# Kernel optimization log

Hardware: AMD Instinct MI355X
Metric: run time of the kernel (lower is better)

Reference implementation:

```python
import jax, jax.numpy as jnp
import numpy as np

B, S, D = 2, 2048, 1024
H = 16
DK = D // H  # 64

def setup_inputs() -> dict:
    key = jax.random.key(0)
    ks = jax.random.split(key, 7)
    scale = 1.0 / np.sqrt(D)
    return {
        "Query": jax.random.normal(ks[0], (B, S, D), dtype=jnp.float32),
        "Key":   jax.random.normal(ks[1], (B, S, D), dtype=jnp.float32),
        "Value": jax.random.normal(ks[2], (B, S, D), dtype=jnp.float32),
        "Wq": jax.random.normal(ks[3], (D, D), dtype=jnp.float32) * scale,
        "Wk": jax.random.normal(ks[4], (D, D), dtype=jnp.float32) * scale,
        "Wv": jax.random.normal(ks[5], (D, D), dtype=jnp.float32) * scale,
        "Wo": jax.random.normal(ks[6], (D, D), dtype=jnp.float32) * scale,
    }

def reference(Query, Key, Value, Wq, Wk, Wv, Wo):
    b = Query.shape[0]
    # nn.Linear(bias=False): x @ W.T ; reshape to [B, H, S, DK]
    q = (Query @ Wq.T).reshape(b, -1, H, DK).transpose(0, 2, 1, 3)
    k = (Key   @ Wk.T).reshape(b, -1, H, DK).transpose(0, 2, 1, 3)
    v = (Value @ Wv.T).reshape(b, -1, H, DK).transpose(0, 2, 1, 3)
    # full O(S^2) score matrix [B, H, Sq, Sk]
    scores = jnp.einsum("bhqd,bhkd->bhqk", q, k) / jnp.sqrt(jnp.float32(DK))
    # FAITHFUL to source: nn.Softmax(dim=1) normalizes over the HEAD axis
    attn = jax.nn.softmax(scores, axis=1)
    ctx = jnp.einsum("bhqk,bhkd->bhqd", attn, v)  # [B, H, Sq, DK]
    ctx = ctx.transpose(0, 2, 1, 3).reshape(b, -1, H * DK)  # [B, S, D]
    return ctx @ Wo.T
```

## Files before the change

### kernel.cpp

```cpp
#include <hip/hip_runtime.h>
#include <stdint.h>

#define BB   2
#define SS   2048
#define DD   1024
#define HH   16
#define DKK  64
#define MM   (BB*SS)

typedef __attribute__((ext_vector_type(4))) float f32x4;
typedef __attribute__((ext_vector_type(8))) short s16x8;

#define MFMA_B16(a, b, c) __builtin_amdgcn_mfma_f32_16x16x32_bf16((a), (b), (c), 0, 0, 0)

__device__ __forceinline__ ushort f2bf(float f) {
  uint u = __float_as_uint(f);
  u += 0x7FFFu + ((u >> 16) & 1u);
  return (ushort)(u >> 16);
}
__device__ __forceinline__ float bf2f(ushort u) {
  return __uint_as_float((uint)u << 16);
}
#if __has_builtin(__builtin_amdgcn_exp2f)
#define EXP2(x) __builtin_amdgcn_exp2f(x)
#else
#define EXP2(x) exp2f(x)
#endif

__device__ __forceinline__ s16x8 cvt8(const float* src) {
  float4 a = *(const float4*)src, b = *(const float4*)(src + 4);
  union { uint u[4]; s16x8 v; } r;
  asm("v_cvt_pk_bf16_f32 %0, %1, %2" : "=v"(r.u[0]) : "v"(a.x), "v"(a.y));
  asm("v_cvt_pk_bf16_f32 %0, %1, %2" : "=v"(r.u[1]) : "v"(a.z), "v"(a.w));
  asm("v_cvt_pk_bf16_f32 %0, %1, %2" : "=v"(r.u[2]) : "v"(b.x), "v"(b.y));
  asm("v_cvt_pk_bf16_f32 %0, %1, %2" : "=v"(r.u[3]) : "v"(b.z), "v"(b.w));
  return r.v;
}

#define QSCALE (0.125f * 1.4426950408889634f)

__global__ void cvt_kernel(const float* __restrict__ src, ushort* __restrict__ dst, int n) {
  int i = (blockIdx.x * 256 + threadIdx.x) * 8;
  if (i >= n) return;
  *(s16x8*)(dst + i) = cvt8(src + i);
}

__global__ __launch_bounds__(256, 2) void qkv_proj(
    const float* __restrict__ Ia, const float* __restrict__ Ib, const float* __restrict__ Ic,
    const ushort* __restrict__ Wa, const ushort* __restrict__ Wb, const ushort* __restrict__ Wc,
    ushort* __restrict__ Oa, ushort* __restrict__ Ob, ushort* __restrict__ Oc)
{
  __shared__ ushort As[128 * 32];
  __shared__ ushort Bs[128 * 32];
  const int tid  = threadIdx.x;
  const int lane = tid & 63, wave = tid >> 6;
  const int q = lane & 15, g = lane >> 4;
  const int wr = wave >> 1, wc = wave & 1;
  const int mblk = blockIdx.x * 128, nblk = blockIdx.y * 128;
  const int mode = blockIdx.z;

  const float*  A = (mode == 0) ? Ia : (mode == 1) ? Ib : Ic;
  const ushort* W = (mode == 0) ? Wa : (mode == 1) ? Wb : Wc;

  f32x4 acc[4][4];
  {
    f32x4 z = {0.f, 0.f, 0.f, 0.f};
#pragma unroll
    for (int i = 0; i < 4; ++i)
#pragma unroll
      for (int j = 0; j < 4; ++j) acc[i][j] = z;
  }

  const int r0 = tid >> 2;
  const int e0 = (tid & 3) * 8;
  for (int k0 = 0; k0 < 1024; k0 += 32) {
#pragma unroll
    for (int it = 0; it < 2; ++it) {
      const int row = r0 + it * 64;
      *(s16x8*)&As[row * 32 + e0] = cvt8(A + (size_t)(mblk + row) * 1024 + k0 + e0);
      *(s16x8*)&Bs[row * 32 + e0] = *(const s16x8*)(W + (size_t)(nblk + row) * 1024 + k0 + e0);
    }
    __syncthreads();
    s16x8 af[4], bf[4];
#pragma unroll
    for (int t = 0; t < 4; ++t) {
      af[t] = *(const s16x8*)&As[(wr * 64 + t * 16 + q) * 32 + g * 8];
      bf[t] = *(const s16x8*)&Bs[(wc * 64 + t * 16 + q) * 32 + g * 8];
    }
#pragma unroll
    for (int mt = 0; mt < 4; ++mt)
#pragma unroll
      for (int nt = 0; nt < 4; ++nt)
        acc[mt][nt] = MFMA_B16(af[mt], bf[nt], acc[mt][nt]);
    __syncthreads();
  }

  if (mode == 2) {
    ushort* Vt = Oc;
#pragma unroll
    for (int mt = 0; mt < 4; ++mt)
#pragma unroll
      for (int nt = 0; nt < 4; ++nt) {
        const int s0 = mblk + wr * 64 + mt * 16 + g * 4;
        const int o  = nblk + wc * 64 + nt * 16 + q;
        const int h = o >> 6, dk = o & 63;
        const int b = s0 >> 11, sr = s0 & 2047;
        ushort4 pk;
        pk.x = f2bf(acc[mt][nt][0]); pk.y = f2bf(acc[mt][nt][1]);
        pk.z = f2bf(acc[mt][nt][2]); pk.w = f2bf(acc[mt][nt][3]);
        *(ushort4*)(Vt + ((size_t)((b * 16 + h) * 64 + dk)) * SS + sr) = pk;
      }
  } else {
    const float scale = (mode == 0) ? QSCALE : 1.0f;
    ushort* P = (mode == 0) ? Oa : Ob;
    ushort* wl = As + wave * 1024;
    const int h0 = (nblk + wc * 64) >> 6;
#pragma unroll
    for (int mt = 0; mt < 4; ++mt) {
      const int s0 = mblk + wr * 64 + mt * 16;
      const int b  = s0 >> 11, sr0 = s0 & 2047;
#pragma unroll
      for (int nt = 0; nt < 4; ++nt)
#pragma unroll
        for (int j = 0; j < 4; ++j)
          wl[(g * 4 + j) * 64 + nt * 16 + q] = f2bf(acc[mt][nt][j] * scale);
#pragma unroll
      for (int it = 0; it < 2; ++it) {
        s16x8 v = *(const s16x8*)((char*)wl + it * 1024 + lane * 16);
        const int lr = it * 8 + (lane >> 3);
        const int c  = (lane & 7) * 8;
        *(s16x8*)(P + ((size_t)((b * 16 + h0) * SS) + sr0 + lr) * DKK + c) = v;
      }
    }
  }
}

__global__ __launch_bounds__(256, 2) void o_proj(
    const ushort* __restrict__ A, const ushort* __restrict__ W,
    float* __restrict__ O)
{
  __shared__ ushort As[128 * 32];
  __shared__ ushort Bs[128 * 32];
  const int tid  = threadIdx.x;
  const int lane = tid & 63, wave = tid >> 6;
  const int q = lane & 15, g = lane >> 4;
  const int wr = wave >> 1, wc = wave & 1;
  const int mblk = blockIdx.x * 128, nblk = blockIdx.y * 128;

  f32x4 acc[4][4];
  {
    f32x4 z = {0.f, 0.f, 0.f, 0.f};
#pragma unroll
    for (int i = 0; i < 4; ++i)
#pragma unroll
      for (int j = 0; j < 4; ++j) acc[i][j] = z;
  }

  const int r0 = tid >> 2;
  const int e0 = (tid & 3) * 8;
  for (int k0 = 0; k0 < 1024; k0 += 32) {
#pragma unroll
    for (int it = 0; it < 2; ++it) {
      const int row = r0 + it * 64;
      *(s16x8*)&As[row * 32 + e0] = *(const s16x8*)(A + (size_t)(mblk + row) * 1024 + k0 + e0);
      *(s16x8*)&Bs[row * 32 + e0] = *(const s16x8*)(W + (size_t)(nblk + row) * 1024 + k0 + e0);
    }
    __syncthreads();
    s16x8 af[4], bf[4];
#pragma unroll
    for (int t = 0; t < 4; ++t) {
      af[t] = *(const s16x8*)&As[(wr * 64 + t * 16 + q) * 32 + g * 8];
      bf[t] = *(const s16x8*)&Bs[(wc * 64 + t * 16 + q) * 32 + g * 8];
    }
#pragma unroll
    for (int mt = 0; mt < 4; ++mt)
#pragma unroll
      for (int nt = 0; nt < 4; ++nt)
        acc[mt][nt] = MFMA_B16(af[mt], bf[nt], acc[mt][nt]);
    __syncthreads();
  }

#pragma unroll
  for (int mt = 0; mt < 4; ++mt)
#pragma unroll
    for (int nt = 0; nt < 4; ++nt)
#pragma unroll
      for (int j = 0; j < 4; ++j) {
        const int s = mblk + wr * 64 + mt * 16 + g * 4 + j;
        const int o = nblk + wc * 64 + nt * 16 + q;
        O[(size_t)s * DD + o] = acc[mt][nt][j];
      }
}

__global__ __launch_bounds__(256, 2) void den_kernel(
    const ushort* __restrict__ Qp, const ushort* __restrict__ Kp,
    ushort* __restrict__ Rden)
{
  __shared__ ushort smem[2][16384];
  const int tid  = threadIdx.x;
  const int lane = tid & 63, wave = tid >> 6;
  const int q = lane & 15, g = lane >> 4;
  const int wr = wave >> 1, wc = wave & 1;
  const int kblk = blockIdx.x * 128, qblk = blockIdx.y * 128;
  const int b = blockIdx.z;

  f32x4 den[4][4];
  {
    f32x4 z = {0.f, 0.f, 0.f, 0.f};
#pragma unroll
    for (int i = 0; i < 4; ++i)
#pragma unroll
      for (int j = 0; j < 4; ++j) den[i][j] = z;
  }

  const int srow = tid >> 3, sseg = tid & 7;
  const int sd   = (sseg * 8) ^ ((srow & 7) << 3);

  const ushort* Kb0 = Kp + ((size_t)(b * 16) * SS + kblk) * DKK;
  const ushort* Qb0 = Qp + ((size_t)(b * 16) * SS + qblk) * DKK;

#pragma unroll
  for (int i = 0; i < 4; ++i) {
    const int row = srow + i * 32;
    *(s16x8*)&smem[0][row * 64 + sd]        = *(const s16x8*)(Kb0 + (size_t)row * DKK + sseg * 8);
    *(s16x8*)&smem[0][8192 + row * 64 + sd] = *(const s16x8*)(Qb0 + (size_t)row * DKK + sseg * 8);
  }
  __syncthreads();

  for (int s = 0; s < 16; ++s) {
    const int cur = s & 1;
    s16x8 nA[4], nB[4];
    if (s < 15) {
      const ushort* Kh = Kb0 + (size_t)(s + 1) * SS * DKK;
      const ushort* Qh = Qb0 + (size_t)(s + 1) * SS * DKK;
#pragma unroll
      for (int i = 0; i < 4; ++i) {
        const int row = srow + i * 32;
        nA[i] = *(const s16x8*)(Kh + (size_t)row * DKK + sseg * 8);
        nB[i] = *(const s16x8*)(Qh + (size_t)row * DKK + sseg * 8);
      }
    }
    s16x8 af[4][2], bf[4][2];
#pragma unroll
    for (int t = 0; t < 4; ++t) {
      const int ra = wr * 64 + t * 16 + q;
      const int rb = wc * 64 + t * 16 + q;
      af[t][0] = *(const s16x8*)&smem[cur][ra * 64 + ((g * 8) ^ ((ra & 7) << 3))];
      af[t][1] = *(const s16x8*)&smem[cur][ra * 64 + ((32 + g * 8) ^ ((ra & 7) << 3))];
      bf[t][0] = *(const s16x8*)&smem[cur][8192 + rb * 64 + ((g * 8) ^ ((rb & 7) << 3))];
      bf[t][1] = *(const s16x8*)&smem[cur][8192 + rb * 64 + ((32 + g * 8) ^ ((rb & 7) << 3))];
    }
#pragma unroll
    for (int mt = 0; mt < 4; ++mt)
#pragma unroll
      for (int nt = 0; nt < 4; ++nt) {
        f32x4 c = {0.f, 0.f, 0.f, 0.f};
        c = MFMA_B16(af[mt][0], bf[nt][0], c);
        c = MFMA_B16(af[mt][1], bf[nt][1], c);
#pragma unroll
        for (int r = 0; r < 4; ++r)
          den[mt][nt][r] += EXP2(c[r]);
      }
    if (s < 15) {
#pragma unroll
      for (int i = 0; i < 4; ++i) {
        const int row = srow + i * 32;
        *(s16x8*)&smem[cur ^ 1][row * 64 + sd]        = nA[i];
        *(s16x8*)&smem[cur ^ 1][8192 + row * 64 + sd] = nB[i];
      }
    }
    __syncthreads();
  }

  char* aw2 = (char*)smem + wave * 8192;
#pragma unroll
  for (int mt = 0; mt < 4; ++mt)
#pragma unroll
    for (int nt = 0; nt < 4; ++nt) {
      const int ql = nt * 16 + q;
      const float i0 = 1.0f / den[mt][nt][0], i1 = 1.0f / den[mt][nt][1];
      const float i2 = 1.0f / den[mt][nt][2], i3 = 1.0f / den[mt][nt][3];
      uint2 pk;
      asm("v_cvt_pk_bf16_f32 %0, %1, %2" : "=v"(pk.x) : "v"(i0), "v"(i1));
      asm("v_cvt_pk_bf16_f32 %0, %1, %2" : "=v"(pk.y) : "v"(i2), "v"(i3));
      *(uint2*)(aw2 + ql * 128 + ((mt * 32 + g * 8) ^ ((ql & 7) << 4))) = pk;
    }
#pragma unroll
  for (int it = 0; it < 8; ++it) {
    const int idx = it * 64 + lane;
    const int row = idx >> 3;
    const int seg = idx & 7;
    s16x8 v = *(const s16x8*)(aw2 + row * 128 + ((seg * 16) ^ ((row & 7) << 4)));
    *(s16x8*)(Rden + (size_t)b * SS * SS
              + (size_t)(qblk + wc * 64 + row) * SS
              + kblk + wr * 64 + seg * 8) = v;
  }
}

__global__ __launch_bounds__(512, 2) void attn5_kernel(
    const ushort* __restrict__ Qp, const ushort* __restrict__ Kp,
    const ushort* __restrict__ Vt, const ushort* __restrict__ Rden,
    ushort* __restrict__ Ctx)
{
  __shared__ ushort Ktile[2][64 * 64];
  __shared__ ushort Vtile[2][64 * 64];
  __shared__ ushort Rw_all[8][16 * 64];
  __shared__ ushort aw_all[8][16 * 64];

  const int tid  = threadIdx.x;
  const int lane = tid & 63;
  const int w    = tid >> 6;
  const int q    = lane & 15;
  const int g    = lane >> 4;
  const int bid  = blockIdx.x;
  const int bh   = bid & 31;
  const int b    = bh >> 4, h = bh & 15;
  const int qblk = (bid >> 5) * 128;

  const ushort* Qb = Qp + ((size_t)bh * SS + qblk + w * 16 + q) * DKK + g * 8;
  s16x8 qf0 = *(const s16x8*)(Qb);
  s16x8 qf1 = *(const s16x8*)(Qb + 32);

  const ushort* Ks = Kp + (size_t)bh * SS * DKK;
  const ushort* Vs = Vt + (size_t)bh * DKK * SS;
  const ushort* Rs = Rden + (size_t)b * SS * SS + (size_t)(qblk + w * 16) * SS;

  f32x4 acc[4];
  {
    f32x4 z = {0.f, 0.f, 0.f, 0.f};
#pragma unroll
    for (int n = 0; n < 4; ++n) acc[n] = z;
  }

  ushort* Rw = Rw_all[w];
  ushort* aw = aw_all[w];
  const int srow = tid >> 3, sseg = tid & 7;
  const int sd   = (sseg * 8) ^ ((srow & 7) << 3);
  const int r16  = lane >> 2;
  const int sgA  = (lane & 3) * 2;
  const int rd0  = r16 * 64 + ((sgA * 8) ^ ((r16 & 7) << 3));
  const int rd1  = r16 * 64 + (((sgA + 1) * 8) ^ ((r16 & 7) << 3));

  {
    s16x8 gK  = *(const s16x8*)(Ks + tid * 8);
    s16x8 gV  = *(const s16x8*)(Vs + (size_t)srow * SS + sseg * 8);
    s16x8 gR0 = *(const s16x8*)(Rs + (size_t)r16 * SS + sgA * 8);
    s16x8 gR1 = *(const s16x8*)(Rs + (size_t)r16 * SS + (sgA + 1) * 8);
    *(s16x8*)&Ktile[0][srow * 64 + sd] = gK;
    *(s16x8*)&Vtile[0][srow * 64 + sd] = gV;
    *(s16x8*)&Rw[rd0] = gR0;
    *(s16x8*)&Rw[rd1] = gR1;
  }
  __syncthreads();

  for (int kt = 0; kt < 32; ++kt) {
    const int cur = kt & 1;
    s16x8 gK, gV, gR0, gR1;
    if (kt < 31) {
      const int k1 = (kt + 1) * 64;
      gK  = *(const s16x8*)(Ks + (size_t)k1 * DKK + tid * 8);
      gV  = *(const s16x8*)(Vs + (size_t)srow * SS + k1 + sseg * 8);
      gR0 = *(const s16x8*)(Rs + (size_t)r16 * SS + k1 + sgA * 8);
      gR1 = *(const s16x8*)(Rs + (size_t)r16 * SS + k1 + (sgA + 1) * 8);
    }
    const ushort* Kt = Ktile[cur];
    const ushort* Vv = Vtile[cur];

#pragma unroll
    for (int ks = 0; ks < 4; ++ks) {
      const int kr = ks * 16 + q;
      s16x8 a0 = *(const s16x8*)&Kt[kr * 64 + ((g * 8) ^ ((kr & 7) << 3))];
      s16x8 a1 = *(const s16x8*)&Kt[kr * 64 + ((32 + g * 8) ^ ((kr & 7) << 3))];
      f32x4 c = {0.f, 0.f, 0.f, 0.f};
      c = MFMA_B16(a0, qf0, c);
      c = MFMA_B16(a1, qf1, c);
      ushort4 rv = *(const ushort4*)&Rw[q * 64 + (((ks * 2 + (g >> 1)) ^ (q & 7)) * 8) + (g & 1) * 4];
      float p0 = EXP2(c[0]) * bf2f(rv.x);
      float p1 = EXP2(c[1]) * bf2f(rv.y);
      float p2 = EXP2(c[2]) * bf2f(rv.z);
      float p3 = EXP2(c[3]) * bf2f(rv.w);
      uint2 pp;
      asm("v_cvt_pk_bf16_f32 %0, %1, %2" : "=v"(pp.x) : "v"(p0), "v"(p1));
      asm("v_cvt_pk_bf16_f32 %0, %1, %2" : "=v"(pp.y) : "v"(p2), "v"(p3));
      *(uint2*)&aw[q * 64 + ((ks * 16 + g * 4) ^ ((q & 7) << 3))] = pp;
    }
#pragma unroll
    for (int kc = 0; kc < 2; ++kc) {
      s16x8 vf[4];
#pragma unroll
      for (int n = 0; n < 4; ++n) {
        const int vr = n * 16 + q;
        vf[n] = *(const s16x8*)&Vv[vr * 64 + ((kc * 32 + g * 8) ^ ((vr & 7) << 3))];
      }
      s16x8 pa = *(const s16x8*)&aw[q * 64 + ((kc * 32 + g * 8) ^ ((q & 7) << 3))];
#pragma unroll
      for (int n = 0; n < 4; ++n)
        acc[n] = MFMA_B16(pa, vf[n], acc[n]);
    }
    if (kt < 31) {
      *(s16x8*)&Ktile[cur ^ 1][srow * 64 + sd] = gK;
      *(s16x8*)&Vtile[cur ^ 1][srow * 64 + sd] = gV;
      *(s16x8*)&Rw[rd0] = gR0;
      *(s16x8*)&Rw[rd1] = gR1;
    }
    __syncthreads();
  }

#pragma unroll
  for (int n = 0; n < 4; ++n)
#pragma unroll
    for (int j = 0; j < 4; ++j)
      aw[(g * 4 + j) * 64 + n * 16 + q] = f2bf(acc[n][j]);
  ushort* P = Ctx + ((size_t)(b * SS) + qblk + w * 16) * DD + h * 64;
#pragma unroll
  for (int it = 0; it < 2; ++it) {
    const int idx = it * 64 + lane;
    const int row = idx >> 3;
    const int seg = idx & 7;
    s16x8 v = *(const s16x8*)&aw[row * 64 + seg * 8];
    *(s16x8*)(P + (size_t)row * DD + seg * 8) = v;
  }
}

extern "C" void kernel_launch(void* const* d_in, const int* in_sizes, int n_in,
                              void* d_out, int out_size, void* d_ws, size_t ws_size,
                              hipStream_t stream) {
  const float* Query = (const float*)d_in[0];
  const float* Key   = (const float*)d_in[1];
  const float* Value = (const float*)d_in[2];
  const float* Wq    = (const float*)d_in[3];
  const float* Wk    = (const float*)d_in[4];
  const float* Wv    = (const float*)d_in[5];
  const float* Wo    = (const float*)d_in[6];

  size_t off = 0;
  char* ws = (char*)d_ws;
  auto alloc = [&](size_t bytes) -> void* {
    void* p = ws + off;
    off += (bytes + 255) & ~(size_t)255;
    return p;
  };
  const size_t nX = (size_t)MM * DD;
  const size_t nW = (size_t)DD * DD;
  const size_t nS = (size_t)BB * SS * SS;
  ushort* Wqb  = (ushort*)alloc(nW * 2);
  ushort* Wkb  = (ushort*)alloc(nW * 2);
  ushort* Wvb  = (ushort*)alloc(nW * 2);
  ushort* Wob  = (ushort*)alloc(nW * 2);
  ushort* Qp   = (ushort*)alloc(nX * 2);
  ushort* Kp   = (ushort*)alloc(nX * 2);
  ushort* Vtb  = (ushort*)alloc(nX * 2);
  ushort* Rden = (ushort*)alloc(nS * 2);
  ushort* Ctx  = (ushort*)alloc(nX * 2);

  cvt_kernel<<<(int)(nW / 2048), 256, 0, stream>>>(Wq, Wqb, (int)nW);
  cvt_kernel<<<(int)(nW / 2048), 256, 0, stream>>>(Wk, Wkb, (int)nW);
  cvt_kernel<<<(int)(nW / 2048), 256, 0, stream>>>(Wv, Wvb, (int)nW);
  cvt_kernel<<<(int)(nW / 2048), 256, 0, stream>>>(Wo, Wob, (int)nW);

  qkv_proj<<<dim3(32, 8, 3), 256, 0, stream>>>(
      Query, Key, Value, Wqb, Wkb, Wvb, Qp, Kp, Vtb);

  den_kernel<<<dim3(16, 16, 2), 256, 0, stream>>>(Qp, Kp, Rden);
  attn5_kernel<<<512, 512, 0, stream>>>(Qp, Kp, Vtb, Rden, Ctx);

  o_proj<<<dim3(32, 8), 256, 0, stream>>>(Ctx, Wob, (float*)d_out);
}
```

Measured before the change: 162.6 us.

## Double-buffer LDS tiles in QKV projection GEMM with register prefetch

The QKV projection main loop now uses two LDS buffers per operand. Global loads for the next K-slice are issued into registers before the MFMAs on the current slice, then converted and stored into the alternate buffer afterward. This hides global memory latency behind compute and removes one barrier per iteration. In exchange it doubles LDS use and raises register pressure, which could hurt occupancy under the 2-blocks-per-CU launch bound.

Measured after the change: 162.8 us. No clear change (+0.1%).

```diff
diff --git a/kernel.cpp b/kernel.cpp
--- a/kernel.cpp
+++ b/kernel.cpp
@@ -27,8 +27,7 @@
 #define EXP2(x) exp2f(x)
 #endif
 
-__device__ __forceinline__ s16x8 cvt8(const float* src) {
-  float4 a = *(const float4*)src, b = *(const float4*)(src + 4);
+__device__ __forceinline__ s16x8 pack8(float4 a, float4 b) {
   union { uint u[4]; s16x8 v; } r;
   asm("v_cvt_pk_bf16_f32 %0, %1, %2" : "=v"(r.u[0]) : "v"(a.x), "v"(a.y));
   asm("v_cvt_pk_bf16_f32 %0, %1, %2" : "=v"(r.u[1]) : "v"(a.z), "v"(a.w));
@@ -36,6 +35,9 @@
   asm("v_cvt_pk_bf16_f32 %0, %1, %2" : "=v"(r.u[3]) : "v"(b.z), "v"(b.w));
   return r.v;
 }
+__device__ __forceinline__ s16x8 cvt8(const float* src) {
+  return pack8(*(const float4*)src, *(const float4*)(src + 4));
+}
 
 #define QSCALE (0.125f * 1.4426950408889634f)
 
@@ -50,8 +52,8 @@
     const ushort* __restrict__ Wa, const ushort* __restrict__ Wb, const ushort* __restrict__ Wc,
     ushort* __restrict__ Oa, ushort* __restrict__ Ob, ushort* __restrict__ Oc)
 {
-  __shared__ ushort As[128 * 32];
-  __shared__ ushort Bs[128 * 32];
+  __shared__ ushort As[2][128 * 32];
+  __shared__ ushort Bs[2][128 * 32];
   const int tid  = threadIdx.x;
   const int lane = tid & 63, wave = tid >> 6;
   const int q = lane & 15, g = lane >> 4;
@@ -73,25 +75,49 @@
 
   const int r0 = tid >> 2;
   const int e0 = (tid & 3) * 8;
-  for (int k0 = 0; k0 < 1024; k0 += 32) {
-#pragma unroll
-    for (int it = 0; it < 2; ++it) {
-      const int row = r0 + it * 64;
-      *(s16x8*)&As[row * 32 + e0] = cvt8(A + (size_t)(mblk + row) * 1024 + k0 + e0);
-      *(s16x8*)&Bs[row * 32 + e0] = *(const s16x8*)(W + (size_t)(nblk + row) * 1024 + k0 + e0);
-    }
-    __syncthreads();
+
+#pragma unroll
+  for (int it = 0; it < 2; ++it) {
+    const int row = r0 + it * 64;
+    *(s16x8*)&As[0][row * 32 + e0] = cvt8(A + (size_t)(mblk + row) * 1024 + e0);
+    *(s16x8*)&Bs[0][row * 32 + e0] = *(const s16x8*)(W + (size_t)(nblk + row) * 1024 + e0);
+  }
+  __syncthreads();
+
+  for (int s = 0; s < 32; ++s) {
+    const int cur = s & 1;
+    float4 fa[2][2];
+    s16x8  wreg[2];
+    if (s < 31) {
+      const int k0 = (s + 1) * 32;
+#pragma unroll
+      for (int it = 0; it < 2; ++it) {
+        const int row = r0 + it * 64;
+        const float* pa = A + (size_t)(mblk + row) * 1024 + k0 + e0;
+        fa[it][0] = *(const float4*)pa;
+        fa[it][1] = *(const float4*)(pa + 4);
+        wreg[it]  = *(const s16x8*)(W + (size_t)(nblk + row) * 1024 + k0 + e0);
+      }
+    }
     s16x8 af[4], bf[4];
 #pragma unroll
     for (int t = 0; t < 4; ++t) {
-      af[t] = *(const s16x8*)&As[(wr * 64 + t * 16 + q) * 32 + g * 8];
-      bf[t] = *(const s16x8*)&Bs[(wc * 64 + t * 16 + q) * 32 + g * 8];
+      af[t] = *(const s16x8*)&As[cur][(wr * 64 + t * 16 + q) * 32 + g * 8];
+      bf[t] = *(const s16x8*)&Bs[cur][(wc * 64 + t * 16 + q) * 32 + g * 8];
     }
 #pragma unroll
     for (int mt = 0; mt < 4; ++mt)
 #pragma unroll
       for (int nt = 0; nt < 4; ++nt)
         acc[mt][nt] = MFMA_B16(af[mt], bf[nt], acc[mt][nt]);
+    if (s < 31) {
+#pragma unroll
+      for (int it = 0; it < 2; ++it) {
+        const int row = r0 + it * 64;
+        *(s16x8*)&As[cur ^ 1][row * 32 + e0] = pack8(fa[it][0], fa[it][1]);
+        *(s16x8*)&Bs[cur ^ 1][row * 32 + e0] = wreg[it];
+      }
+    }
     __syncthreads();
   }
 
@@ -113,7 +139,7 @@
   } else {
     const float scale = (mode == 0) ? QSCALE : 1.0f;
     ushort* P = (mode == 0) ? Oa : Ob;
-    ushort* wl = As + wave * 1024;
+    ushort* wl = &As[0][wave * 1024];
     const int h0 = (nblk + wc * 64) >> 6;
 #pragma unroll
     for (int mt = 0; mt < 4; ++mt) {
```
